# Kernel tuning notes

Measured on AMD Instinct MI355X. Metric: run time of the kernel, lower is better.

## Reference

```python
import jax, jax.numpy as jnp
import numpy as np
import math

B, S, D_IN, D, H, L, NC = 4, 2048, 64, 512, 8, 2, 2
DK = D // H
FACTOR = 5
TOPK = min(FACTOR * int(math.log(S)), S)  # 35
EPS = 1e-5


def make_pe():
    # sinusoidal positional encoding [S, D]
    pos = jnp.arange(S, dtype=jnp.float32)[:, None]
    div = jnp.exp(jnp.arange(0, D, 2, dtype=jnp.float32) * (-math.log(10000.0) / D))
    pe = jnp.zeros((S, D), jnp.float32)
    pe = pe.at[:, 0::2].set(jnp.sin(pos * div)).at[:, 1::2].set(jnp.cos(pos * div))
    return pe


def layernorm(x, g, b):
    m = x.mean(-1, keepdims=True)
    v = x.var(-1, keepdims=True)
    return (x - m) / jnp.sqrt(v + EPS) * g + b


def setup_inputs() -> dict:
    key = jax.random.key(0)
    ks = iter(jax.random.split(key, 16))
    def p(shape, s=0.02):
        return jax.random.normal(next(ks), shape, jnp.float32) * s
    return dict(
        x=jax.random.normal(next(ks), (B, S, D_IN), jnp.float32),
        emb_w=p((D_IN, D)), emb_b=jnp.zeros((D,), jnp.float32),
        wq=p((L, D, D)), bq=jnp.zeros((L, D), jnp.float32),
        wk=p((L, D, D)), bk=jnp.zeros((L, D), jnp.float32),
        wv=p((L, D, D)), bv=jnp.zeros((L, D), jnp.float32),
        wo=p((L, D, D)), bo=jnp.zeros((L, D), jnp.float32),
        ff1_w=p((L, D, 4 * D)), ff1_b=jnp.zeros((L, 4 * D), jnp.float32),
        ff2_w=p((L, 4 * D, D)), ff2_b=jnp.zeros((L, D), jnp.float32),
        ln1_g=jnp.ones((L, D), jnp.float32), ln1_b=jnp.zeros((L, D), jnp.float32),
        ln2_g=jnp.ones((L, D), jnp.float32), ln2_b=jnp.zeros((L, D), jnp.float32),
        dec1_w=p((D, D // 2)), dec1_b=jnp.zeros((D // 2,), jnp.float32),
        dec2_w=p((D // 2, NC)), dec2_b=jnp.zeros((NC,), jnp.float32),
    )


def reference(x, emb_w, emb_b, wq, bq, wk, bk, wv, bv, wo, bo,
              ff1_w, ff1_b, ff2_w, ff2_b, ln1_g, ln1_b, ln2_g, ln2_b,
              dec1_w, dec1_b, dec2_w, dec2_b):
    h = x @ emb_w + emb_b + make_pe()[None]  # [B,S,D]
    scale = 1.0 / math.sqrt(DK)
    for i in range(L):
        q = (h @ wq[i] + bq[i]).reshape(B, S, H, DK).transpose(0, 2, 1, 3)
        k = (h @ wk[i] + bk[i]).reshape(B, S, H, DK).transpose(0, 2, 1, 3)
        v = (h @ wv[i] + bv[i]).reshape(B, S, H, DK).transpose(0, 2, 1, 3)
        scores = jnp.einsum('bhqd,bhkd->bhqk', q, k) * scale  # [B,H,S,S]
        top_scores, _ = jax.lax.top_k(scores, TOPK)            # [B,H,S,TOPK]
        attn = jax.nn.softmax(top_scores, axis=-1)
        # NOTE: faithful to source quirk — V sliced to its FIRST TOPK rows,
        # top_indices are discarded by the original module.
        ao = jnp.einsum('bhqk,bhkd->bhqd', attn, v[:, :, :TOPK, :])
        ao = ao.transpose(0, 2, 1, 3).reshape(B, S, D) @ wo[i] + bo[i]
        h = layernorm(h + ao, ln1_g[i], ln1_b[i])
        ff = jax.nn.relu(h @ ff1_w[i] + ff1_b[i]) @ ff2_w[i] + ff2_b[i]
        h = layernorm(h + ff, ln2_g[i], ln2_b[i])
    pooled = h.mean(axis=1)  # AdaptiveAvgPool1d(1) over seq
    out = jax.nn.relu(pooled @ dec1_w + dec1_b) @ dec2_w + dec2_b  # [B,NC]
    return out
```

## Files before the change

kernel.cpp:

```cpp
#include <hip/hip_runtime.h>
#include <cmath>

typedef unsigned short u16;
typedef __attribute__((ext_vector_type(8))) short short8;
typedef __attribute__((ext_vector_type(4))) float float4v;
typedef unsigned short ushort2v __attribute__((ext_vector_type(2)));

#define S_LEN 2048
#define NTOK  8192
#define TOPK  35
#define NT512 ((size_t)NTOK*512)

__device__ __forceinline__ u16 f2b(float f){
  unsigned int x = __float_as_uint(f);
  unsigned int r = (x + 0x7fffu + ((x >> 16) & 1u)) >> 16;
  return (u16)r;
}

__device__ __forceinline__ unsigned key_of(float f){
  unsigned u = (unsigned)f2b(f);
  unsigned m = (u & 0x8000u) ? 0xFFFFu : 0x8000u;
  return (u ^ m) & 0xFFFFu;
}
__device__ __forceinline__ float key_to_f(unsigned key){
  unsigned m = (key & 0x8000u) ? 0x8000u : 0xFFFFu;
  return __uint_as_float(((key ^ m) & 0xFFFFu) << 16);
}
__device__ __forceinline__ unsigned key2_of(unsigned u){
  unsigned t = (u >> 15) & 0x00010001u;
  unsigned mask = 0x80008000u + (t << 15) - t;
  return u ^ mask;
}
__device__ __forceinline__ unsigned pkmax(unsigned a, unsigned b){
  union { unsigned u; ushort2v v; } x, y, r;
  x.u = a; y.u = b;
  r.v = __builtin_elementwise_max(x.v, y.v);
  return r.u;
}
__device__ __forceinline__ unsigned pkmin(unsigned a, unsigned b){
  union { unsigned u; ushort2v v; } x, y, r;
  x.u = a; y.u = b;
  r.v = __builtin_elementwise_min(x.v, y.v);
  return r.u;
}

__device__ __forceinline__ void bsort128(unsigned &v0, unsigned &v1, int l){
  #pragma unroll
  for (int k = 2; k <= 128; k <<= 1){
    #pragma unroll
    for (int j = k >> 1; j > 0; j >>= 1){
      if (j == 64){
        unsigned hi = pkmax(v0, v1), lo = pkmin(v0, v1);
        v0 = hi; v1 = lo;
      } else {
        unsigned o0 = (unsigned)__shfl_xor((int)v0, j, 64);
        unsigned o1 = (unsigned)__shfl_xor((int)v1, j, 64);
        bool up0 = (((l & k) == 0) != ((l & j) != 0));
        bool up1 = ((((64 + l) & k) == 0) != ((l & j) != 0));
        unsigned hi0 = pkmax(v0, o0), lo0 = pkmin(v0, o0);
        unsigned hi1 = pkmax(v1, o1), lo1 = pkmin(v1, o1);
        v0 = up0 ? hi0 : lo0;
        v1 = up1 ? hi1 : lo1;
      }
    }
  }
}

__device__ __forceinline__ void gload16(const void* g, void* l){
  __builtin_amdgcn_global_load_lds(
      (const __attribute__((address_space(1))) unsigned int*)g,
      (__attribute__((address_space(3))) unsigned int*)l, 16, 0, 0);
}

struct WtArgs {
  const float* wq; const float* wk; const float* wv; const float* wo;
  const float* ff1w; const float* ff2w;
  u16* wt_qkv; u16* wt_wo; u16* wt_ff1; u16* wt_ff2;
};
__global__ void prep_kernel(WtArgs a,
                            const float* __restrict__ x, const float* __restrict__ w,
                            const float* __restrict__ bias, float* __restrict__ h,
                            u16* __restrict__ h16){
  __shared__ float xs[4][64];
  __shared__ u16 t[32][33];
  int bx = blockIdx.x;
  int tid = threadIdx.x;
  if (bx < 6144){
    int l  = (bx >= 3072) ? 1 : 0;
    int tt = bx - l*3072;
    const float* W; u16* Wt; int K, N, tx_, ty_;
    if (tt < 1024){
      int seg = tt >> 8, r = tt & 255;
      tx_ = r & 15; ty_ = r >> 4; K = 512; N = 512;
      if (seg == 0){ W = a.wq + (size_t)l*262144; Wt = a.wt_qkv + (size_t)l*786432; }
      else if (seg == 1){ W = a.wk + (size_t)l*262144; Wt = a.wt_qkv + (size_t)l*786432 + 262144; }
      else if (seg == 2){ W = a.wv + (size_t)l*262144; Wt = a.wt_qkv + (size_t)l*786432 + 524288; }
      else { W = a.wo + (size_t)l*262144; Wt = a.wt_wo + (size_t)l*262144; }
    } else if (tt < 2048){
      int r = tt - 1024;
      tx_ = r & 63; ty_ = r >> 6; K = 512; N = 2048;
      W = a.ff1w + (size_t)l*1048576; Wt = a.wt_ff1 + (size_t)l*1048576;
    } else {
      int r = tt - 2048;
      tx_ = r & 15; ty_ = r >> 4; K = 2048; N = 512;
      W = a.ff2w + (size_t)l*1048576; Wt = a.wt_ff2 + (size_t)l*1048576;
    }
    int k0 = ty_*32, n0 = tx_*32;
    int tx = tid & 31, ty = tid >> 5;
    #pragma unroll
    for (int i = ty; i < 32; i += 8)
      t[i][tx] = f2b(W[(size_t)(k0+i)*N + n0+tx]);
    __syncthreads();
    #pragma unroll
    for (int i = ty; i < 32; i += 8)
      Wt[(size_t)(n0+i)*K + k0+tx] = t[tx][i];
  } else {
    int t0 = (bx - 6144) * 4;
    xs[tid >> 6][tid & 63] = x[(size_t)(t0 + (tid >> 6))*64 + (tid & 63)];
    __syncthreads();
    float b0 = bias[tid], b1 = bias[tid + 256];
    float acc[4][2];
    #pragma unroll
    for (int tk = 0; tk < 4; ++tk){ acc[tk][0] = b0; acc[tk][1] = b1; }
    #pragma unroll 8
    for (int k = 0; k < 64; ++k){
      float w0 = w[k*512 + tid];
      float w1 = w[k*512 + tid + 256];
      #pragma unroll
      for (int tk = 0; tk < 4; ++tk){
        float xv = xs[tk][k];
        acc[tk][0] += xv * w0;
        acc[tk][1] += xv * w1;
      }
    }
    const float neg_ln1e4_over_D = -9.210340371976184f / 512.f;
    int c0 = tid, c1 = tid + 256;
    float e0 = expf((float)(c0 & ~1) * neg_ln1e4_over_D);
    float e1 = expf((float)(c1 & ~1) * neg_ln1e4_over_D);
    #pragma unroll
    for (int tk = 0; tk < 4; ++tk){
      int tok = t0 + tk;
      int s = tok & (S_LEN - 1);
      float a0 = (float)s * e0;
      float p0 = (c0 & 1) ? cosf(a0) : sinf(a0);
      float a1 = (float)s * e1;
      float p1 = (c1 & 1) ? cosf(a1) : sinf(a1);
      float v0 = acc[tk][0] + p0, v1 = acc[tk][1] + p1;
      h[(size_t)tok*512 + c0] = v0;  h16[(size_t)tok*512 + c0] = f2b(v0);
      h[(size_t)tok*512 + c1] = v1;  h16[(size_t)tok*512 + c1] = f2b(v1);
    }
  }
}

template<int EPI, int DBUF>
__global__ __launch_bounds__(256) void gemm_mfma(
    const u16* __restrict__ A, int lda, const u16* __restrict__ Bt, int ldb,
    const float* __restrict__ bias0, const float* __restrict__ bias1,
    const float* __restrict__ bias2,
    float* __restrict__ Cf, u16* __restrict__ C16a, u16* __restrict__ C16b,
    float* __restrict__ Cv, int M, int N, int Klen){
  __shared__ __align__(16) u16 As[(DBUF ? 2 : 1)*128*64];
  __shared__ __align__(16) u16 Bs[(DBUF ? 2 : 1)*128*64];
  int tid = threadIdx.x;
  int w = tid >> 6, l = tid & 63, quad = l >> 4, m = l & 15;
  int gx = gridDim.x;
  int orig = blockIdx.y * gx + blockIdx.x;
  int nwg  = gx * gridDim.y;
  int tt   = (orig & 7) * (nwg >> 3) + (orig >> 3);
  int m0 = (tt / gx) * 128, n0 = (tt % gx) * 128;
  int mh = (w >> 1)*64, nh = (w & 1)*64;
  float4v acc[4][4];
  #pragma unroll
  for (int i = 0; i < 4; ++i)
    #pragma unroll
    for (int j = 0; j < 4; ++j) acc[i][j] = (float4v){0.f,0.f,0.f,0.f};

  #define GSTAGE(ofs, kt) do { \
    _Pragma("unroll") \
    for (int c = 0; c < 4; ++c){ \
      int g = c*256 + tid; \
      int row = g >> 3, scx = g & 7, dc = scx ^ (row & 7); \
      gload16(A  + (size_t)(m0+row)*lda + (kt) + dc*8, As + (ofs) + (size_t)g*8); \
      gload16(Bt + (size_t)(n0+row)*ldb + (kt) + dc*8, Bs + (ofs) + (size_t)g*8); \
    } } while(0)

  #define GCOMPUTE(Ac, Bc) do { \
    _Pragma("unroll") \
    for (int kk = 0; kk < 2; ++kk){ \
      short8 af[4], bf[4]; \
      _Pragma("unroll") \
      for (int i = 0; i < 4; ++i){ \
        int dcx = kk*4 + quad; \
        int ra = mh + i*16 + m; \
        af[i] = *(const short8*)((Ac) + (size_t)(ra*8 + (dcx ^ (ra & 7)))*8); \
        int rb = nh + i*16 + m; \
        bf[i] = *(const short8*)((Bc) + (size_t)(rb*8 + (dcx ^ (rb & 7)))*8); \
      } \
      _Pragma("unroll") \
      for (int i = 0; i < 4; ++i) \
        _Pragma("unroll") \
        for (int j = 0; j < 4; ++j) \
          acc[i][j] = __builtin_amdgcn_mfma_f32_16x16x32_bf16(af[i], bf[j], acc[i][j], 0, 0, 0); \
    } } while(0)

  if (DBUF){
    GSTAGE(0, 0);
    __syncthreads();
    int cur = 0;
    for (int kt = 0; kt < Klen; kt += 64){
      int nxt = cur ^ 1;
      if (kt + 64 < Klen) GSTAGE(nxt*(128*64), kt + 64);
      GCOMPUTE(As + cur*(128*64), Bs + cur*(128*64));
      __syncthreads();
      cur = nxt;
    }
  } else {
    for (int kt = 0; kt < Klen; kt += 64){
      GSTAGE(0, kt);
      __syncthreads();
      GCOMPUTE(As, Bs);
      __syncthreads();
    }
  }
  #undef GSTAGE
  #undef GCOMPUTE

  #pragma unroll
  for (int i = 0; i < 4; ++i){
    #pragma unroll
    for (int j = 0; j < 4; ++j){
      int col = n0 + nh + j*16 + m;
      #pragma unroll
      for (int r = 0; r < 4; ++r){
        int row = m0 + mh + i*16 + quad*4 + r;
        float v = acc[i][j][r];
        if (EPI == 0){
          Cf[(size_t)row*N + col] = v + bias0[col];
        } else if (EPI == 1){
          C16a[(size_t)row*N + col] = f2b(fmaxf(v + bias0[col], 0.f));
        } else {
          int sel = col >> 9, n5 = col & 511;
          const float* bp = (sel == 0) ? bias0 : (sel == 1) ? bias1 : bias2;
          float vv = v + bp[n5];
          int d = n5 & 63, hh = n5 >> 6;
          int b = row >> 11, s = row & 2047;
          size_t idx = (((size_t)(b*8 + hh))*2048 + s)*64 + d;
          if (sel == 0)      C16a[idx] = f2b(vv);
          else if (sel == 1) C16b[idx] = f2b(vv);
          else if (s < TOPK) Cv[idx]  = vv;
        }
      }
    }
  }
}

__global__ __launch_bounds__(512, 8) void attn_mfma_topk(
    const u16* __restrict__ qb16, const u16* __restrict__ kb16,
    const float* __restrict__ vb, u16* __restrict__ aob16){
  __shared__ unsigned pr[8*1024];
  int tid  = threadIdx.x;
  int w    = tid >> 6, l = tid & 63;
  int quad = l >> 4,  m = l & 15;
  int orig = blockIdx.y * 128 + blockIdx.x;
  int t4   = ((orig & 7) << 9) | (orig >> 3);
  int bh   = t4 >> 7;
  int q0   = (t4 & 127) << 4;

  const u16* Qp = qb16 + ((size_t)bh*2048 + q0 + m)*64 + quad*8;
  short8 a0 = *(const short8*)Qp;
  short8 a1 = *(const short8*)(Qp + 32);

  const u16* Kbase = kb16 + (size_t)bh*2048*64;
  unsigned sc[32];
  int swz = (quad & 1) << 4;
  const u16* kp0 = Kbase + (size_t)(w*128 + m)*64 + quad*8;
  const uint4* p4 = (const uint4*)(pr + w*1024);

  short8 cb0 = *(const short8*)kp0;
  short8 cb1 = *(const short8*)(kp0 + 32);
  #pragma unroll
  for (int t = 0; t < 16; ++t){
    short8 nb0, nb1;
    if (t < 15){
      int tn = t + 1;
      const u16* np = kp0 + (size_t)(((tn >> 3) << 10) + ((tn & 7) << 4))*64;
      nb0 = *(const short8*)np;
      nb1 = *(const short8*)(np + 32);
    }
    float4v acc = {0.f, 0.f, 0.f, 0.f};
    acc = __builtin_amdgcn_mfma_f32_16x16x32_bf16(a0, cb0, acc, 0, 0, 0);
    acc = __builtin_amdgcn_mfma_f32_16x16x32_bf16(a1, cb1, acc, 0, 0, 0);
    int lk = (w << 7) + ((t & 7) << 4);
    #pragma unroll
    for (int c = 0; c < 2; ++c){
      unsigned xa = __float_as_uint(acc[2*c]);
      unsigned xb = __float_as_uint(acc[2*c+1]);
      unsigned ta = xa + 0x7fffu + ((xa >> 16) & 1u);
      unsigned tb = xb + 0x7fffu + ((xb >> 16) & 1u);
      unsigned pk = (ta >> 16) | (tb & 0xFFFF0000u);
      pr[(quad*2 + c)*1024 + ((lk + m) ^ swz)] = key2_of(pk);
    }
    cb0 = nb0; cb1 = nb1;
    if (t == 7){
      __syncthreads();
      #pragma unroll
      for (int j = 0; j < 4; ++j){
        uint4 v4 = p4[j*64 + l];
        sc[j*4+0] = v4.x; sc[j*4+1] = v4.y; sc[j*4+2] = v4.z; sc[j*4+3] = v4.w;
      }
      __syncthreads();
    }
  }
  __syncthreads();
  #pragma unroll
  for (int j = 0; j < 4; ++j){
    uint4 v4 = p4[j*64 + l];
    sc[16+j*4+0] = v4.x; sc[16+j*4+1] = v4.y; sc[16+j*4+2] = v4.z; sc[16+j*4+3] = v4.w;
  }

  unsigned* row = &pr[w*1024];

  unsigned m1 = pkmax(sc[0], sc[1]);
  unsigned m2 = pkmin(sc[0], sc[1]);
  #pragma unroll
  for (int i = 2; i < 32; ++i){
    unsigned v = sc[i];
    unsigned nm1 = pkmax(m1, v);
    m2 = pkmax(m2, pkmin(m1, v));
    m1 = nm1;
  }

  unsigned mA1 = m1 & 0xFFFFu, mB1 = m1 >> 16;
  unsigned mA2 = m2 & 0xFFFFu, mB2 = m2 >> 16;
  unsigned tA = 0, tB = 0;
  #pragma unroll
  for (int bit = 15; bit >= 0; --bit){
    unsigned cA = tA | (1u << bit);
    unsigned cB = tB | (1u << bit);
    int nA = __popcll(__ballot(mA1 >= cA)) + __popcll(__ballot(mA2 >= cA));
    int nB = __popcll(__ballot(mB1 >= cB)) + __popcll(__ballot(mB2 >= cB));
    if (nA >= TOPK) tA = cA;
    if (nB >= TOPK) tB = cB;
  }
  unsigned TT = (tA - 1) | ((tB - 1) << 16);

  unsigned mask = 0;
  #pragma unroll
  for (int i = 0; i < 32; ++i){
    mask |= (pkmax(sc[i], TT) != TT) ? (1u << i) : 0u;
  }
  int cnt = __popc(mask);

  int pre = cnt;
  #pragma unroll
  for (int off = 1; off < 64; off <<= 1){
    int n = __shfl_up(pre, off, 64);
    if (l >= off) pre += n;
  }
  pre -= cnt;

  #pragma unroll
  for (int i = 0; i < 32; ++i){
    if (mask & (1u << i)){
      int p = pre + __popc(mask & ((1u << i) - 1u));
      if (p < 128) row[p] = sc[i];
    }
  }
  int tot = __shfl(pre + cnt, 63, 64);

  unsigned c0 = (l < tot)      ? row[l]      : 0u;
  unsigned c1 = (64 + l < tot) ? row[64 + l] : 0u;

  const float* Vb = vb + (size_t)bh*2048*64 + l;
  float vreg[TOPK];
  #pragma unroll
  for (int r = 0; r < TOPK; ++r) vreg[r] = Vb[(size_t)r*64];

  bsort128(c0, c1, l);

  unsigned top0 = (unsigned)__shfl((int)c0, 0, 64);
  float mAf = key_to_f(top0 & 0xFFFFu) * 0.125f;
  float mBf = key_to_f(top0 >> 16)     * 0.125f;
  float tvA = key_to_f(c0 & 0xFFFFu)   * 0.125f;
  float tvB = key_to_f(c0 >> 16)       * 0.125f;
  float wAv = (l < TOPK) ? __expf(tvA - mAf) : 0.f;
  float wBv = (l < TOPK) ? __expf(tvB - mBf) : 0.f;

  float dA = wAv, dB = wBv;
  #pragma unroll
  for (int off = 32; off > 0; off >>= 1){
    dA += __shfl_xor(dA, off, 64);
    dB += __shfl_xor(dB, off, 64);
  }

  float accA = 0.f, accB = 0.f;
  #pragma unroll
  for (int r = 0; r < TOPK; ++r){
    float wA = __uint_as_float((unsigned)__builtin_amdgcn_readlane((int)__float_as_uint(wAv), r));
    float wB = __uint_as_float((unsigned)__builtin_amdgcn_readlane((int)__float_as_uint(wBv), r));
    float vv = vreg[r];
    accA += wA * vv;
    accB += wB * vv;
  }
  accA *= __builtin_amdgcn_rcpf(dA);
  accB *= __builtin_amdgcn_rcpf(dB);

  int b = bh >> 3, hh = bh & 7;
  int sA = q0 + w*2;
  aob16[(((size_t)(b*2048 + sA))*8 + hh)*64 + l]     = f2b(accA);
  aob16[(((size_t)(b*2048 + sA + 1))*8 + hh)*64 + l] = f2b(accB);
}

__global__ void resid_ln_kernel(float* __restrict__ h, const float* __restrict__ t,
                                const float* __restrict__ g, const float* __restrict__ b,
                                u16* __restrict__ h16){
  int half = threadIdx.x >> 7;
  int tok  = blockIdx.x*2 + half;
  int tid  = threadIdx.x & 127;
  size_t base4 = (size_t)tok * 128;
  float4 hv = ((const float4*)h)[base4 + tid];
  float4 tv = ((const float4*)t)[base4 + tid];
  float x0 = hv.x + tv.x, x1 = hv.y + tv.y;
  float x2 = hv.z + tv.z, x3 = hv.w + tv.w;
  __shared__ float red[8];
  int wid = threadIdx.x >> 6, lane = threadIdx.x & 63;

  float s = (x0 + x1) + (x2 + x3);
  #pragma unroll
  for (int off = 32; off > 0; off >>= 1) s += __shfl_xor(s, off, 64);
  if (lane == 0) red[wid] = s;
  __syncthreads();
  int hb = half << 1;
  float mean = (red[hb] + red[hb+1]) * (1.f/512.f);

  float d0 = x0 - mean, d1 = x1 - mean, d2 = x2 - mean, d3 = x3 - mean;
  float sq = (d0*d0 + d1*d1) + (d2*d2 + d3*d3);
  #pragma unroll
  for (int off = 32; off > 0; off >>= 1) sq += __shfl_xor(sq, off, 64);
  if (lane == 0) red[4 + wid] = sq;
  __syncthreads();
  float var = (red[4 + hb] + red[4 + hb + 1]) * (1.f/512.f);
  float inv = rsqrtf(var + 1e-5f);
  float4 gv = ((const float4*)g)[tid];
  float4 bv = ((const float4*)b)[tid];
  float o0 = d0 * inv * gv.x + bv.x;
  float o1 = d1 * inv * gv.y + bv.y;
  float o2 = d2 * inv * gv.z + bv.z;
  float o3 = d3 * inv * gv.w + bv.w;
  ((float4*)h)[base4 + tid] = make_float4(o0, o1, o2, o3);
  if (h16){
    uint2 pk;
    pk.x = (unsigned)f2b(o0) | ((unsigned)f2b(o1) << 16);
    pk.y = (unsigned)f2b(o2) | ((unsigned)f2b(o3) << 16);
    ((uint2*)h16)[base4 + tid] = pk;
  }
}

__global__ void pool_kernel(const float* __restrict__ h, float* __restrict__ part){
  int c = blockIdx.x * 256 + threadIdx.x;
  int b = blockIdx.y;
  int z = blockIdx.z;
  const float* p = h + ((size_t)b * 2048 + z * 64) * 512 + c;
  float acc = 0.f;
  #pragma unroll 8
  for (int s = 0; s < 64; ++s) acc += p[(size_t)s * 512];
  part[((size_t)(z*4 + b))*512 + c] = acc;
}

__global__ void decoder_kernel(const float* __restrict__ part,
                               const float* __restrict__ w1, const float* __restrict__ b1,
                               const float* __restrict__ w2, const float* __restrict__ b2,
                               float* __restrict__ out){
  __shared__ float ps[4][512];
  __shared__ float hid[4][256];
  int tid = threadIdx.x;
  for (int i = tid; i < 2048; i += 256){
    int b = i >> 9, c = i & 511;
    float s = 0.f;
    #pragma unroll
    for (int z = 0; z < 32; ++z) s += part[((size_t)(z*4 + b))*512 + c];
    ps[b][c] = s * (1.f/2048.f);
  }
  __syncthreads();
  float bb = b1[tid];
  for (int b = 0; b < 4; ++b){
    float acc = bb;
    for (int k = 0; k < 512; ++k) acc += ps[b][k] * w1[k*256 + tid];
    hid[b][tid] = fmaxf(acc, 0.f);
  }
  __syncthreads();
  if (tid < 8){
    int b = tid >> 1, c = tid & 1;
    float acc = b2[c];
    for (int j = 0; j < 256; ++j) acc += hid[b][j] * w2[j*2 + c];
    out[b*2 + c] = acc;
  }
}

extern "C" void kernel_launch(void* const* d_in, const int* in_sizes, int n_in,
                              void* d_out, int out_size, void* d_ws, size_t ws_size,
                              hipStream_t stream){
  const float* x     = (const float*)d_in[0];
  const float* emb_w = (const float*)d_in[1];
  const float* emb_b = (const float*)d_in[2];
  const float* wq    = (const float*)d_in[3];
  const float* bq    = (const float*)d_in[4];
  const float* wk    = (const float*)d_in[5];
  const float* bk    = (const float*)d_in[6];
  const float* wv    = (const float*)d_in[7];
  const float* bv    = (const float*)d_in[8];
  const float* wo    = (const float*)d_in[9];
  const float* bo    = (const float*)d_in[10];
  const float* ff1w  = (const float*)d_in[11];
  const float* ff1b  = (const float*)d_in[12];
  const float* ff2w  = (const float*)d_in[13];
  const float* ff2b  = (const float*)d_in[14];
  const float* ln1g  = (const float*)d_in[15];
  const float* ln1b  = (const float*)d_in[16];
  const float* ln2g  = (const float*)d_in[17];
  const float* ln2b  = (const float*)d_in[18];
  const float* d1w   = (const float*)d_in[19];
  const float* d1b   = (const float*)d_in[20];
  const float* d2w   = (const float*)d_in[21];
  const float* d2b   = (const float*)d_in[22];

  float* h      = (float*)d_ws;
  float* tmp    = h + NT512;
  u16*   u      = (u16*)(tmp + NT512);
  u16*   h16    = u;
  u16*   q16    = u + NT512;
  u16*   k16    = u + 2*NT512;
  float* vb     = (float*)(u + 3*NT512);
  u16*   ff16   = q16;
  u16*   aob16  = (u16*)(vb + NT512);
  u16*   wt     = aob16 + NT512;
  u16*   wt_qkv = wt;
  u16*   wt_wo  = wt_qkv + (size_t)2*1536*512;
  u16*   wt_ff1 = wt_wo  + (size_t)2*512*512;
  u16*   wt_ff2 = wt_ff1 + (size_t)2*2048*512;
  float* part   = tmp;

  WtArgs wa{wq, wk, wv, wo, ff1w, ff2w, wt_qkv, wt_wo, wt_ff1, wt_ff2};
  prep_kernel<<<8192, 256, 0, stream>>>(wa, x, emb_w, emb_b, h, h16);

  for (int l = 0; l < 2; ++l){
    gemm_mfma<2, 0><<<dim3(12, 64), 256, 0, stream>>>(
        h16, 512, wt_qkv + (size_t)l*1536*512, 512,
        bq + l*512, bk + l*512, bv + l*512,
        nullptr, q16, k16, vb, NTOK, 1536, 512);

    attn_mfma_topk<<<dim3(128, 32), 512, 0, stream>>>(q16, k16, vb, aob16);

    gemm_mfma<0, 1><<<dim3(4, 64), 256, 0, stream>>>(
        aob16, 512, wt_wo + (size_t)l*512*512, 512,
        bo + l*512, nullptr, nullptr,
        tmp, nullptr, nullptr, nullptr, NTOK, 512, 512);
    resid_ln_kernel<<<NTOK/2, 256, 0, stream>>>(h, tmp, ln1g + l*512, ln1b + l*512, h16);

    gemm_mfma<1, 0><<<dim3(16, 64), 256, 0, stream>>>(
        h16, 512, wt_ff1 + (size_t)l*2048*512, 512,
        ff1b + l*2048, nullptr, nullptr,
        nullptr, ff16, nullptr, nullptr, NTOK, 2048, 512);

    gemm_mfma<0, 1><<<dim3(4, 64), 256, 0, stream>>>(
        ff16, 2048, wt_ff2 + (size_t)l*512*2048, 2048,
        ff2b + l*512, nullptr, nullptr,
        tmp, nullptr, nullptr, nullptr, NTOK, 512, 2048);
    resid_ln_kernel<<<NTOK/2, 256, 0, stream>>>(h, tmp, ln2g + l*512, ln2b + l*512,
                                                (l == 1) ? nullptr : h16);
  }

  pool_kernel<<<dim3(2, 4, 32), 256, 0, stream>>>(h, part);
  decoder_kernel<<<1, 256, 0, stream>>>(part, d1w, d1b, d2w, d2b, (float*)d_out);
}
```

Before: 689.3 us.

## Halve attention block to 4 waves, each wave handling four query rows

The top-k attention kernel now launches 256 threads instead of 512. Each wave scores 256 keys per pass and performs the threshold search, compaction, sort and softmax-weighted V sum for four query rows instead of two. The same tile is covered with fewer waves, so per-wave setup such as the Q loads, the V register preload of 35 rows and the scans is amortised over more rows. In exchange, register pressure roughly doubles and fewer waves are available to hide latency, and the shared buffer stays at 32 KB for a smaller block.

```diff
diff --git a/kernel.cpp b/kernel.cpp
--- a/kernel.cpp
+++ b/kernel.cpp
@@ -17,11 +17,6 @@
   return (u16)r;
 }
 
-__device__ __forceinline__ unsigned key_of(float f){
-  unsigned u = (unsigned)f2b(f);
-  unsigned m = (u & 0x8000u) ? 0xFFFFu : 0x8000u;
-  return (u ^ m) & 0xFFFFu;
-}
 __device__ __forceinline__ float key_to_f(unsigned key){
   unsigned m = (key & 0x8000u) ? 0x8000u : 0xFFFFu;
   return __uint_as_float(((key ^ m) & 0xFFFFu) << 16);
@@ -254,7 +249,7 @@
   }
 }
 
-__global__ __launch_bounds__(512, 8) void attn_mfma_topk(
+__global__ __launch_bounds__(256, 4) void attn_mfma_topk(
     const u16* __restrict__ qb16, const u16* __restrict__ kb16,
     const float* __restrict__ vb, u16* __restrict__ aob16){
   __shared__ unsigned pr[8*1024];
@@ -271,26 +266,27 @@
   short8 a1 = *(const short8*)(Qp + 32);
 
   const u16* Kbase = kb16 + (size_t)bh*2048*64;
-  unsigned sc[32];
+  unsigned scA[32], scB[32];
   int swz = (quad & 1) << 4;
-  const u16* kp0 = Kbase + (size_t)(w*128 + m)*64 + quad*8;
-  const uint4* p4 = (const uint4*)(pr + w*1024);
+  const u16* kp0 = Kbase + (size_t)(w*256 + m)*64 + quad*8;
+  const uint4* p4a = (const uint4*)(pr + (2*w)*1024);
+  const uint4* p4b = (const uint4*)(pr + (2*w+1)*1024);
 
   short8 cb0 = *(const short8*)kp0;
   short8 cb1 = *(const short8*)(kp0 + 32);
   #pragma unroll
-  for (int t = 0; t < 16; ++t){
+  for (int t = 0; t < 32; ++t){
     short8 nb0, nb1;
-    if (t < 15){
+    if (t < 31){
       int tn = t + 1;
-      const u16* np = kp0 + (size_t)(((tn >> 3) << 10) + ((tn & 7) << 4))*64;
+      const u16* np = kp0 + (size_t)(((tn >> 4) << 10) + ((tn & 15) << 4))*64;
       nb0 = *(const short8*)np;
       nb1 = *(const short8*)(np + 32);
     }
     float4v acc = {0.f, 0.f, 0.f, 0.f};
     acc = __builtin_amdgcn_mfma_f32_16x16x32_bf16(a0, cb0, acc, 0, 0, 0);
     acc = __builtin_amdgcn_mfma_f32_16x16x32_bf16(a1, cb1, acc, 0, 0, 0);
-    int lk = (w << 7) + ((t & 7) << 4);
+    int lk = (w << 8) + ((t & 15) << 4);
     #pragma unroll
     for (int c = 0; c < 2; ++c){
       unsigned xa = __float_as_uint(acc[2*c]);
@@ -301,12 +297,14 @@
       pr[(quad*2 + c)*1024 + ((lk + m) ^ swz)] = key2_of(pk);
     }
     cb0 = nb0; cb1 = nb1;
-    if (t == 7){
+    if (t == 15){
       __syncthreads();
       #pragma unroll
       for (int j = 0; j < 4; ++j){
-        uint4 v4 = p4[j*64 + l];
-        sc[j*4+0] = v4.x; sc[j*4+1] = v4.y; sc[j*4+2] = v4.z; sc[j*4+3] = v4.w;
+        uint4 va = p4a[j*64 + l];
+        scA[j*4+0] = va.x; scA[j*4+1] = va.y; scA[j*4+2] = va.z; scA[j*4+3] = va.w;
+        uint4 vb_ = p4b[j*64 + l];
+        scB[j*4+0] = vb_.x; scB[j*4+1] = vb_.y; scB[j*4+2] = vb_.z; scB[j*4+3] = vb_.w;
       }
       __syncthreads();
     }
@@ -314,62 +312,85 @@
   __syncthreads();
   #pragma unroll
   for (int j = 0; j < 4; ++j){
-    uint4 v4 = p4[j*64 + l];
-    sc[16+j*4+0] = v4.x; sc[16+j*4+1] = v4.y; sc[16+j*4+2] = v4.z; sc[16+j*4+3] = v4.w;
-  }
-
-  unsigned* row = &pr[w*1024];
-
-  unsigned m1 = pkmax(sc[0], sc[1]);
-  unsigned m2 = pkmin(sc[0], sc[1]);
+    uint4 va = p4a[j*64 + l];
+    scA[16+j*4+0] = va.x; scA[16+j*4+1] = va.y; scA[16+j*4+2] = va.z; scA[16+j*4+3] = va.w;
+    uint4 vb_ = p4b[j*64 + l];
+    scB[16+j*4+0] = vb_.x; scB[16+j*4+1] = vb_.y; scB[16+j*4+2] = vb_.z; scB[16+j*4+3] = vb_.w;
+  }
+
+  unsigned* rowA = &pr[(2*w)*1024];
+  unsigned* rowB = &pr[(2*w+1)*1024];
+
+  unsigned m1a = pkmax(scA[0], scA[1]), m2a = pkmin(scA[0], scA[1]);
+  unsigned m1b = pkmax(scB[0], scB[1]), m2b = pkmin(scB[0], scB[1]);
   #pragma unroll
   for (int i = 2; i < 32; ++i){
-    unsigned v = sc[i];
-    unsigned nm1 = pkmax(m1, v);
-    m2 = pkmax(m2, pkmin(m1, v));
-    m1 = nm1;
-  }
-
-  unsigned mA1 = m1 & 0xFFFFu, mB1 = m1 >> 16;
-  unsigned mA2 = m2 & 0xFFFFu, mB2 = m2 >> 16;
-  unsigned tA = 0, tB = 0;
+    unsigned va = scA[i];
+    unsigned na = pkmax(m1a, va);
+    m2a = pkmax(m2a, pkmin(m1a, va));
+    m1a = na;
+    unsigned vb_ = scB[i];
+    unsigned nb_ = pkmax(m1b, vb_);
+    m2b = pkmax(m2b, pkmin(m1b, vb_));
+    m1b = nb_;
+  }
+
+  unsigned a1h = m1a & 0xFFFFu, a1H = m1a >> 16;
+  unsigned a2h = m2a & 0xFFFFu, a2H = m2a >> 16;
+  unsigned b1h = m1b & 0xFFFFu, b1H = m1b >> 16;
+  unsigned b2h = m2b & 0xFFFFu, b2H = m2b >> 16;
+  unsigned tA = 0, tB = 0, tC = 0, tD = 0;
   #pragma unroll
   for (int bit = 15; bit >= 0; --bit){
-    unsigned cA = tA | (1u << bit);
-    unsigned cB = tB | (1u << bit);
-    int nA = __popcll(__ballot(mA1 >= cA)) + __popcll(__ballot(mA2 >= cA));
-    int nB = __popcll(__ballot(mB1 >= cB)) + __popcll(__ballot(mB2 >= cB));
+    unsigned cA = tA | (1u << bit), cB = tB | (1u << bit);
+    unsigned cC = tC | (1u << bit), cD = tD | (1u << bit);
+    int nA = __popcll(__ballot(a1h >= cA)) + __popcll(__ballot(a2h >= cA));
+    int nB = __popcll(__ballot(a1H >= cB)) + __popcll(__ballot(a2H >= cB));
+    int nC = __popcll(__ballot(b1h >= cC)) + __popcll(__ballot(b2h >= cC));
+    int nD = __popcll(__ballot(b1H >= cD)) + __popcll(__ballot(b2H >= cD));
     if (nA >= TOPK) tA = cA;
     if (nB >= TOPK) tB = cB;
-  }
-  unsigned TT = (tA - 1) | ((tB - 1) << 16);
-
-  unsigned mask = 0;
+    if (nC >= TOPK) tC = cC;
+    if (nD >= TOPK) tD = cD;
+  }
+  unsigned TTa = (tA - 1) | ((tB - 1) << 16);
+  unsigned TTb = (tC - 1) | ((tD - 1) << 16);
+
+  unsigned maskA = 0, maskB = 0;
   #pragma unroll
   for (int i = 0; i < 32; ++i){
-    mask |= (pkmax(sc[i], TT) != TT) ? (1u << i) : 0u;
-  }
-  int cnt = __popc(mask);
-
-  int pre = cnt;
+    maskA |= (pkmax(scA[i], TTa) != TTa) ? (1u << i) : 0u;
+    maskB |= (pkmax(scB[i], TTb) != TTb) ? (1u << i) : 0u;
+  }
+  int cntA = __popc(maskA), cntB = __popc(maskB);
+
+  int preA = cntA, preB = cntB;
   #pragma unroll
   for (int off = 1; off < 64; off <<= 1){
-    int n = __shfl_up(pre, off, 64);
-    if (l >= off) pre += n;
-  }
-  pre -= cnt;
+    int nA_ = __shfl_up(preA, off, 64);
+    int nB_ = __shfl_up(preB, off, 64);
+    if (l >= off){ preA += nA_; preB += nB_; }
+  }
+  preA -= cntA; preB -= cntB;
 
   #pragma unroll
   for (int i = 0; i < 32; ++i){
-    if (mask & (1u << i)){
-      int p = pre + __popc(mask & ((1u << i) - 1u));
-      if (p < 128) row[p] = sc[i];
-    }
-  }
-  int tot = __shfl(pre + cnt, 63, 64);
-
-  unsigned c0 = (l < tot)      ? row[l]      : 0u;
-  unsigned c1 = (64 + l < tot) ? row[64 + l] : 0u;
+    if (maskA & (1u << i)){
+      int p = preA + __popc(maskA & ((1u << i) - 1u));
+      if (p < 128) rowA[p] = scA[i];
+    }
+    if (maskB & (1u << i)){
+      int p = preB + __popc(maskB & ((1u << i) - 1u));
+      if (p < 128) rowB[p] = scB[i];
+    }
+  }
+  int totA = __shfl(preA + cntA, 63, 64);
+  int totB = __shfl(preB + cntB, 63, 64);
+
+  unsigned c0 = (l < totA)      ? rowA[l]      : 0u;
+  unsigned c1 = (64 + l < totA) ? rowA[64 + l] : 0u;
+  unsigned c2 = (l < totB)      ? rowB[l]      : 0u;
+  unsigned c3 = (64 + l < totB) ? rowB[64 + l] : 0u;
 
   const float* Vb = vb + (size_t)bh*2048*64 + l;
   float vreg[TOPK];
@@ -377,38 +398,57 @@
   for (int r = 0; r < TOPK; ++r) vreg[r] = Vb[(size_t)r*64];
 
   bsort128(c0, c1, l);
-
-  unsigned top0 = (unsigned)__shfl((int)c0, 0, 64);
-  float mAf = key_to_f(top0 & 0xFFFFu) * 0.125f;
-  float mBf = key_to_f(top0 >> 16)     * 0.125f;
-  float tvA = key_to_f(c0 & 0xFFFFu)   * 0.125f;
-  float tvB = key_to_f(c0 >> 16)       * 0.125f;
-  float wAv = (l < TOPK) ? __expf(tvA - mAf) : 0.f;
-  float wBv = (l < TOPK) ? __expf(tvB - mBf) : 0.f;
-
-  float dA = wAv, dB = wBv;
+  bsort128(c2, c3, l);
+
+  unsigned topA = (unsigned)__shfl((int)c0, 0, 64);
+  unsigned topB = (unsigned)__shfl((int)c2, 0, 64);
+  float mA = key_to_f(topA & 0xFFFFu) * 0.125f;
+  float mB = key_to_f(topA >> 16)     * 0.125f;
+  float mC = key_to_f(topB & 0xFFFFu) * 0.125f;
+  float mD = key_to_f(topB >> 16)     * 0.125f;
+  float vA = key_to_f(c0 & 0xFFFFu)   * 0.125f;
+  float vB = key_to_f(c0 >> 16)       * 0.125f;
+  float vC = key_to_f(c2 & 0xFFFFu)   * 0.125f;
+  float vD = key_to_f(c2 >> 16)       * 0.125f;
+  bool in = (l < TOPK);
+  float wA = in ? __expf(vA - mA) : 0.f;
+  float wB = in ? __expf(vB - mB) : 0.f;
+  float wC = in ? __expf(vC - mC) : 0.f;
+  float wD = in ? __expf(vD - mD) : 0.f;
+
+  float dA = wA, dB = wB, dC = wC, dD = wD;
   #pragma unroll
   for (int off = 32; off > 0; off >>= 1){
     dA += __shfl_xor(dA, off, 64);
     dB += __shfl_xor(dB, off, 64);
-  }
-
-  float accA = 0.f, accB = 0.f;
+    dC += __shfl_xor(dC, off, 64);
+    dD += __shfl_xor(dD, off, 64);
+  }
+
+  float oA = 0.f, oB = 0.f, oC = 0.f, oD = 0.f;
   #pragma unroll
   for (int r = 0; r < TOPK; ++r){
-    float wA = __uint_as_float((unsigned)__builtin_amdgcn_readlane((int)__float_as_uint(wAv), r));
-    float wB = __uint_as_float((unsigned)__builtin_amdgcn_readlane((int)__float_as_uint(wBv), r));
+    float rA = __uint_as_float((unsigned)__builtin_amdgcn_readlane((int)__float_as_uint(wA), r));
+    float rB = __uint_as_float((unsigned)__builtin_amdgcn_readlane((int)__float_as_uint(wB), r));
+    float rC = __uint_as_float((unsigned)__builtin_amdgcn_readlane((int)__float_as_uint(wC), r));
+    float rD = __uint_as_float((unsigned)__builtin_amdgcn_readlane((int)__float_as_uint(wD), r));
     float vv = vreg[r];
-    accA += wA * vv;
-    accB += wB * vv;
-  }
-  accA *= __builtin_amdgcn_rcpf(dA);
-  accB *= __builtin_amdgcn_rcpf(dB);
+    oA += rA * vv;
+    oB += rB * vv;
+    oC += rC * vv;
+    oD += rD * vv;
+  }
+  oA *= __builtin_amdgcn_rcpf(dA);
+  oB *= __builtin_amdgcn_rcpf(dB);
+  oC *= __builtin_amdgcn_rcpf(dC);
+  oD *= __builtin_amdgcn_rcpf(dD);
 
   int b = bh >> 3, hh = bh & 7;
-  int sA = q0 + w*2;
-  aob16[(((size_t)(b*2048 + sA))*8 + hh)*64 + l]     = f2b(accA);
-  aob16[(((size_t)(b*2048 + sA + 1))*8 + hh)*64 + l] = f2b(accB);
+  int sA = q0 + 4*w;
+  aob16[(((size_t)(b*2048 + sA))*8 + hh)*64 + l]     = f2b(oA);
+  aob16[(((size_t)(b*2048 + sA + 1))*8 + hh)*64 + l] = f2b(oB);
+  aob16[(((size_t)(b*2048 + sA + 2))*8 + hh)*64 + l] = f2b(oC);
+  aob16[(((size_t)(b*2048 + sA + 3))*8 + hh)*64 + l] = f2b(oD);
 }
 
 __global__ void resid_ln_kernel(float* __restrict__ h, const float* __restrict__ t,
@@ -549,7 +589,7 @@
         bq + l*512, bk + l*512, bv + l*512,
         nullptr, q16, k16, vb, NTOK, 1536, 512);
 
-    attn_mfma_topk<<<dim3(128, 32), 512, 0, stream>>>(q16, k16, vb, aob16);
+    attn_mfma_topk<<<dim3(128, 32), 256, 0, stream>>>(q16, k16, vb, aob16);
 
     gemm_mfma<0, 1><<<dim3(4, 64), 256, 0, stream>>>(
         aob16, 512, wt_wo + (size_t)l*512*512, 512,
```

Result: no change. 680.7 us, median of 3 (-1.2%).
